# Performance work log

Hardware: AMD Instinct MI355X
Metric: run time of the kernel (lower is better)

The kernel has to match this reference:

```python
import jax, jax.numpy as jnp
import numpy as np


def setup_inputs() -> dict:
    key = jax.random.key(0)
    ks = jax.random.split(key, 7)
    B, T, C, H = 4, 4096, 1024, 64
    x = jax.random.normal(ks[0], (B, T, C), dtype=jnp.float32)
    Wq = jax.random.normal(ks[1], (C, H), dtype=jnp.float32) * 0.02
    bq = jax.random.normal(ks[2], (H,), dtype=jnp.float32) * 0.02
    Wk = jax.random.normal(ks[3], (C, H), dtype=jnp.float32) * 0.02
    bk = jax.random.normal(ks[4], (H,), dtype=jnp.float32) * 0.02
    Wv = jax.random.normal(ks[5], (C, H), dtype=jnp.float32) * 0.02
    bv = jax.random.normal(ks[6], (H,), dtype=jnp.float32) * 0.02
    return {"x": x, "Wq": Wq, "bq": bq, "Wk": Wk, "bk": bk, "Wv": Wv, "bv": bv}


def reference(x, Wq, bq, Wk, bk, Wv, bv):
    B, T, C = x.shape
    q = x @ Wq + bq            # [B,T,H]
    k = x @ Wk + bk            # [B,T,H]
    v = x @ Wv + bv            # [B,T,H]
    # NOTE: original scales by C**-0.5 where C = n_embd (input dim), not head_size
    scale = jnp.asarray(C, x.dtype) ** -0.5
    wei = jnp.einsum('bth,bsh->bts', q, k) * scale   # [B,T,T]
    causal = jnp.tril(jnp.ones((T, T), dtype=bool))
    wei = jnp.where(causal, wei, -jnp.inf)
    wei = jax.nn.softmax(wei, axis=-1)
    out = jnp.einsum('bts,bsh->bth', wei, v)         # [B,T,H]
    return out
```

## Files before the change

### kernel.cpp

```cpp
#include <hip/hip_runtime.h>
#include <hip/hip_bf16.h>

#define T_DIM 4096
#define C_DIM 1024
#define H_DIM 64
#define B_DIM 4

typedef __attribute__((ext_vector_type(8))) short short8v;
typedef __attribute__((ext_vector_type(4))) short short4v;
typedef __attribute__((ext_vector_type(4))) float float4v;

__device__ __forceinline__ unsigned short f2bf(float f) {
    __hip_bfloat16 h = __float2bfloat16(f);
    return *reinterpret_cast<unsigned short*>(&h);
}

__device__ __forceinline__ int vperm(int t5) {
    return ((t5 & 12) << 1) | (t5 & 3) | ((t5 & 16) >> 2);
}

#define GLL16(gsrc, ldst)                                                         \
    __builtin_amdgcn_global_load_lds(                                             \
        (const __attribute__((address_space(1))) unsigned int*)(gsrc),            \
        (__attribute__((address_space(3))) unsigned int*)(ldst), 16, 0, 0)

__global__ __launch_bounds__(256) void wprep(
    const float* __restrict__ Wq, const float* __restrict__ Wk,
    const float* __restrict__ Wv, unsigned short* __restrict__ wt)
{
    __shared__ float tile[64][65];
    const int t  = threadIdx.x;
    const int m  = blockIdx.x >> 4;
    const int k0 = (blockIdx.x & 15) * 64;
    const float* __restrict__ W = (m == 0) ? Wq : (m == 1) ? Wk : Wv;

    const int kr = t >> 4, c4 = (t & 15) * 4;
#pragma unroll
    for (int j = 0; j < 4; ++j) {
        const int row = kr + j * 16;
        const float4 v = *(const float4*)(W + (size_t)(k0 + row) * 64 + c4);
        tile[row][c4 + 0] = v.x; tile[row][c4 + 1] = v.y;
        tile[row][c4 + 2] = v.z; tile[row][c4 + 3] = v.w;
    }
    __syncthreads();

    const int col = t >> 2, q = t & 3;
    short8v s0, s1;
#pragma unroll
    for (int j = 0; j < 8; ++j) s0[j] = (short)f2bf(tile[q * 16 + j][col]);
#pragma unroll
    for (int j = 0; j < 8; ++j) s1[j] = (short)f2bf(tile[q * 16 + 8 + j][col]);
    unsigned short* dst = wt + (size_t)(m * 64 + col) * 1024 + k0 + q * 16;
    *(short8v*)dst = s0;
    *(short8v*)(dst + 8) = s1;
}

__global__ __launch_bounds__(512, 2) void qkv_gemm(
    const float* __restrict__ x, const unsigned short* __restrict__ wt,
    const float* __restrict__ bq, const float* __restrict__ bk,
    const float* __restrict__ bv,
    unsigned short* __restrict__ qb, unsigned short* __restrict__ kmat,
    unsigned short* __restrict__ vP)
{
    __shared__ __align__(16) unsigned char lx[2][4096];
    __shared__ __align__(16) unsigned char lw[2][24576];

    const int t    = threadIdx.x;
    const int lane = t & 63;
    const int w    = t >> 6;
    const int l15  = lane & 15;
    const int g4   = lane >> 4;
    const int r0   = blockIdx.x * 32;

    const int rg  = w & 1;
    const int cgr = (w >> 1) & 1;
    const int kh  = w >> 2;

    const int srow  = t >> 3;
    const int soct  = t & 7;
    const int sphys = soct ^ (srow & 7);
    const float* __restrict__ xsrc = x + (size_t)(r0 + srow) * C_DIM + soct * 8;
    const int wgs = (t & 7) ^ ((t >> 3) & 7);
    const unsigned char* __restrict__ wB = (const unsigned char*)wt;

    float4v acc[6];
#pragma unroll
    for (int cg = 0; cg < 6; ++cg) acc[cg] = (float4v){0.f, 0.f, 0.f, 0.f};

#define WSTAGE(p, kb)                                                             \
    {                                                                             \
        _Pragma("unroll")                                                         \
        for (int i = 0; i < 3; ++i)                                               \
            GLL16(wB + (size_t)(i * 64 + (t >> 3)) * 2048 + (kb) * 128 + wgs * 16,\
                  &lw[p][(i * 512 + t) * 16]);                                    \
    }

    WSTAGE(0, 0);
    if (t < 256) {
        const float4 a0 = *(const float4*)(xsrc);
        const float4 a1 = *(const float4*)(xsrc + 4);
        short8v xs;
        xs[0] = (short)f2bf(a0.x); xs[1] = (short)f2bf(a0.y);
        xs[2] = (short)f2bf(a0.z); xs[3] = (short)f2bf(a0.w);
        xs[4] = (short)f2bf(a1.x); xs[5] = (short)f2bf(a1.y);
        xs[6] = (short)f2bf(a1.z); xs[7] = (short)f2bf(a1.w);
        *(short8v*)&lx[0][srow * 128 + sphys * 16] = xs;
    }
    __syncthreads();

    const int arow = rg * 16 + l15;
    const int axor = arow & 7;
    const int kg   = kh * 4 + g4;

    for (int kb = 0; kb < 16; ++kb) {
        const int p = kb & 1;
        float4 na = {0,0,0,0}, nb = {0,0,0,0};
        if (kb < 15) {
            if (t < 256) {
                na = *(const float4*)(xsrc + (kb + 1) * 64);
                nb = *(const float4*)(xsrc + (kb + 1) * 64 + 4);
            }
            WSTAGE(p ^ 1, kb + 1);
        }

        const short8v af = *(const short8v*)&lx[p][arow * 128 + (kg ^ axor) * 16];
#pragma unroll
        for (int cg = 0; cg < 6; ++cg) {
            const int col = cgr * 96 + cg * 16 + l15;
            const short8v bf =
                *(const short8v*)&lw[p][col * 128 + ((kg ^ (col & 7))) * 16];
            acc[cg] = __builtin_amdgcn_mfma_f32_16x16x32_bf16(af, bf, acc[cg], 0, 0, 0);
        }

        if (kb < 15 && t < 256) {
            short8v xs;
            xs[0] = (short)f2bf(na.x); xs[1] = (short)f2bf(na.y);
            xs[2] = (short)f2bf(na.z); xs[3] = (short)f2bf(na.w);
            xs[4] = (short)f2bf(nb.x); xs[5] = (short)f2bf(nb.y);
            xs[6] = (short)f2bf(nb.z); xs[7] = (short)f2bf(nb.w);
            *(short8v*)&lx[p ^ 1][srow * 128 + sphys * 16] = xs;
        }
        __syncthreads();
    }

    float* comm = (float*)lw;
    if (kh == 1) {
        const int base = ((w - 4) * 64 + lane) * 24;
#pragma unroll
        for (int cg = 0; cg < 6; ++cg)
#pragma unroll
            for (int e = 0; e < 4; ++e) comm[base + cg * 4 + e] = acc[cg][e];
    }
    __syncthreads();
    if (kh == 0) {
        const int base = (w * 64 + lane) * 24;
#pragma unroll
        for (int cg = 0; cg < 6; ++cg)
#pragma unroll
            for (int e = 0; e < 4; ++e) acc[cg][e] += comm[base + cg * 4 + e];

        const float qs = 0.03125f * 1.44269504088896f;
#pragma unroll
        for (int cg = 0; cg < 6; ++cg) {
            const int cabs = cgr * 96 + cg * 16 + l15;
            const int m    = cabs >> 6;
            const int h    = cabs & 63;
            const float bb = ((m == 0) ? bq : (m == 1) ? bk : bv)[h];
#pragma unroll
            for (int rr = 0; rr < 4; ++rr) {
                const int row = r0 + rg * 16 + 4 * g4 + rr;
                const float vv = acc[cg][rr] + bb;
                if (m == 0) {
                    qb[(size_t)row * 64 + h] = f2bf(vv * qs);
                } else if (m == 1) {
                    kmat[(size_t)row * 64 + h] = f2bf(vv);
                } else {
                    const int b_i = row >> 12;
                    const int tt  = row & 4095;
                    const int tp  = (tt & ~31) | vperm(tt & 31);
                    vP[((size_t)b_i * 64 + h) * T_DIM + tp] = f2bf(vv);
                }
            }
        }
    }
#undef WSTAGE
}

__global__ __launch_bounds__(512, 4) void attn_mfma(
    const unsigned short* __restrict__ qb, const unsigned short* __restrict__ kmat,
    const unsigned short* __restrict__ vP, float* __restrict__ out)
{
    __shared__ float partO[8][32][68];
    __shared__ float partl[8][32];

    const int w    = threadIdx.x >> 6;
    const int lane = threadIdx.x & 63;
    const int l15  = lane & 15;
    const int g    = lane >> 4;
    const int i    = blockIdx.x;
    const int p2   = (i & 255) >> 2;
    const int b    = i & 3;
    const int tt   = (i < 256) ? (127 - p2) : p2;
    const int q0   = tt * 32;
    const int n    = tt + 1;

    const unsigned short* __restrict__ qbase = qb + ((size_t)b * T_DIM + q0) * 64;
    short8v qf[2][2];
    qf[0][0] = *(const short8v*)(qbase + (size_t)l15 * 64 + 8 * g);
    qf[0][1] = *(const short8v*)(qbase + (size_t)l15 * 64 + 32 + 8 * g);
    qf[1][0] = *(const short8v*)(qbase + (size_t)(16 + l15) * 64 + 8 * g);
    qf[1][1] = *(const short8v*)(qbase + (size_t)(16 + l15) * 64 + 32 + 8 * g);

    const unsigned short* __restrict__ kbase = kmat + (size_t)b * T_DIM * 64;
    const unsigned short* __restrict__ vbase = vP + (size_t)b * 64 * T_DIM;

    float4v acc[2][4];
#pragma unroll
    for (int qt = 0; qt < 2; ++qt)
#pragma unroll
        for (int f = 0; f < 4; ++f) acc[qt][f] = (float4v){0.f, 0.f, 0.f, 0.f};
    float lsum[2] = {0.f, 0.f};

    const int rem = n & 7;
    const int cnt = (n >> 3) + (w < rem ? 1 : 0);
    const int st  = w * (n >> 3) + (w < rem ? w : rem);

    for (int s = 0; s < cnt; ++s) {
        const int kv0 = (st + s) * 32;

        const unsigned short* kr0 = kbase + (size_t)(kv0 + l15) * 64 + 8 * g;
        const unsigned short* kr1 = kr0 + 16 * 64;
        const short8v ka0 = *(const short8v*)kr0;
        const short8v ka1 = *(const short8v*)(kr0 + 32);
        const short8v ka2 = *(const short8v*)kr1;
        const short8v ka3 = *(const short8v*)(kr1 + 32);

        short8v vb4[4];
#pragma unroll
        for (int f = 0; f < 4; ++f)
            vb4[f] = *(const short8v*)(
                vbase + (size_t)(f * 16 + l15) * T_DIM + kv0 + 8 * g);

#pragma unroll
        for (int qt = 0; qt < 2; ++qt) {
            const float4v z = (float4v){0.f, 0.f, 0.f, 0.f};
            float4v slo = __builtin_amdgcn_mfma_f32_16x16x32_bf16(ka0, qf[qt][0], z, 0, 0, 0);
            slo = __builtin_amdgcn_mfma_f32_16x16x32_bf16(ka1, qf[qt][1], slo, 0, 0, 0);
            float4v shi = __builtin_amdgcn_mfma_f32_16x16x32_bf16(ka2, qf[qt][0], z, 0, 0, 0);
            shi = __builtin_amdgcn_mfma_f32_16x16x32_bf16(ka3, qf[qt][1], shi, 0, 0, 0);

            short8v pa;
            float ls = 0.f;
            if (kv0 + 31 <= q0 + 16 * qt) {
#pragma unroll
                for (int r = 0; r < 4; ++r) {
                    const float plo = exp2f(slo[r]);
                    const float phi = exp2f(shi[r]);
                    pa[r]     = (short)f2bf(plo);
                    pa[4 + r] = (short)f2bf(phi);
                    ls += plo + phi;
                }
            } else {
                const int qabs = q0 + 16 * qt + l15;
#pragma unroll
                for (int r = 0; r < 4; ++r) {
                    const int kvlo = kv0 + 4 * g + r;
                    const float plo = (kvlo <= qabs) ? exp2f(slo[r]) : 0.f;
                    const float phi = (kvlo + 16 <= qabs) ? exp2f(shi[r]) : 0.f;
                    pa[r]     = (short)f2bf(plo);
                    pa[4 + r] = (short)f2bf(phi);
                    ls += plo + phi;
                }
            }
            lsum[qt] += ls;
#pragma unroll
            for (int f = 0; f < 4; ++f)
                acc[qt][f] = __builtin_amdgcn_mfma_f32_16x16x32_bf16(pa, vb4[f], acc[qt][f], 0, 0, 0);
        }
    }

#pragma unroll
    for (int qt = 0; qt < 2; ++qt) {
        lsum[qt] += __shfl_xor(lsum[qt], 16);
        lsum[qt] += __shfl_xor(lsum[qt], 32);
    }

#pragma unroll
    for (int qt = 0; qt < 2; ++qt)
#pragma unroll
        for (int f = 0; f < 4; ++f)
#pragma unroll
            for (int r = 0; r < 4; ++r)
                partO[w][16 * qt + 4 * g + r][16 * f + l15] = acc[qt][f][r];
    if (g == 0) {
        partl[w][l15]      = lsum[0];
        partl[w][16 + l15] = lsum[1];
    }
    __syncthreads();

    const int row = threadIdx.x >> 4;
    const int c0  = (threadIdx.x & 15) * 4;
    float lt = 0.f;
#pragma unroll
    for (int ww = 0; ww < 8; ++ww) lt += partl[ww][row];
    const float inv = 1.f / lt;
    float4 o = make_float4(0.f, 0.f, 0.f, 0.f);
#pragma unroll
    for (int ww = 0; ww < 8; ++ww) {
        const float4 s = *(const float4*)&partO[ww][row][c0];
        o.x += s.x; o.y += s.y; o.z += s.z; o.w += s.w;
    }
    o.x *= inv; o.y *= inv; o.z *= inv; o.w *= inv;
    *(float4*)(out + ((size_t)b * T_DIM + q0 + row) * 64 + c0) = o;
}

extern "C" void kernel_launch(void* const* d_in, const int* in_sizes, int n_in,
                              void* d_out, int out_size, void* d_ws, size_t ws_size,
                              hipStream_t stream) {
    const float* x  = (const float*)d_in[0];
    const float* Wq = (const float*)d_in[1];
    const float* bq = (const float*)d_in[2];
    const float* Wk = (const float*)d_in[3];
    const float* bk = (const float*)d_in[4];
    const float* Wv = (const float*)d_in[5];
    const float* bv = (const float*)d_in[6];
    float* out = (float*)d_out;

    const size_t rows = (size_t)B_DIM * T_DIM;
    char* ws = (char*)d_ws;
    unsigned short* qb   = (unsigned short*)ws;
    unsigned short* kmat = qb + rows * H_DIM;
    unsigned short* vP   = kmat + rows * H_DIM;
    unsigned short* wt   = vP + rows * H_DIM;

    wprep<<<48, 256, 0, stream>>>(Wq, Wk, Wv, wt);
    qkv_gemm<<<512, 512, 0, stream>>>(x, wt, bq, bk, bv, qb, kmat, vP);
    attn_mfma<<<512, 512, 0, stream>>>(qb, kmat, vP, out);
}
```

Measured before the change: 63.02 us.

## Pipeline x loads in projection with all threads; compute softmax row sums via MFMA

The projection kernel now has all 512 threads load and convert x in float4 pieces. It prefetches two k-steps ahead with alternating registers, uses packed bf16 conversions and replaces __syncthreads with explicit waitcnt/barrier plus sched_barriers. The k-loop is fully unrolled and the last iteration is peeled. In the attention kernel, the per-row probability sum moves from scalar adds plus cross-lane shuffles to an extra MFMA against a ones vector, and the probabilities are packed with paired bf16 conversion. The aim is more overlap of memory latency and fewer VALU instructions, at the cost of one more MFMA per tile and row sums taken from bf16-rounded probabilities, which changes numerics slightly.

```diff
diff --git a/kernel.cpp b/kernel.cpp
--- a/kernel.cpp
+++ b/kernel.cpp
@@ -76,10 +76,10 @@
     const int cgr = (w >> 1) & 1;
     const int kh  = w >> 2;
 
-    const int srow  = t >> 3;
-    const int soct  = t & 7;
-    const int sphys = soct ^ (srow & 7);
-    const float* __restrict__ xsrc = x + (size_t)(r0 + srow) * C_DIM + soct * 8;
+    const int srow  = t >> 4;
+    const int sq    = t & 15;
+    const int xbyte = srow * 128 + ((sq >> 1) ^ (srow & 7)) * 16 + (sq & 1) * 8;
+    const float* __restrict__ xsrc = x + (size_t)(r0 + srow) * C_DIM + sq * 4;
     const int wgs = (t & 7) ^ ((t >> 3) & 7);
     const unsigned char* __restrict__ wB = (const unsigned char*)wt;
 
@@ -94,34 +94,40 @@
             GLL16(wB + (size_t)(i * 64 + (t >> 3)) * 2048 + (kb) * 128 + wgs * 16,\
                   &lw[p][(i * 512 + t) * 16]);                                    \
     }
-
-    WSTAGE(0, 0);
-    if (t < 256) {
-        const float4 a0 = *(const float4*)(xsrc);
-        const float4 a1 = *(const float4*)(xsrc + 4);
-        short8v xs;
-        xs[0] = (short)f2bf(a0.x); xs[1] = (short)f2bf(a0.y);
-        xs[2] = (short)f2bf(a0.z); xs[3] = (short)f2bf(a0.w);
-        xs[4] = (short)f2bf(a1.x); xs[5] = (short)f2bf(a1.y);
-        xs[6] = (short)f2bf(a1.z); xs[7] = (short)f2bf(a1.w);
-        *(short8v*)&lx[0][srow * 128 + sphys * 16] = xs;
-    }
-    __syncthreads();
+#define XCVT_WRITE(p, v)                                                          \
+    {                                                                             \
+        __hip_bfloat162 c0_ = __float22bfloat162_rn(make_float2((v).x, (v).y));   \
+        __hip_bfloat162 c1_ = __float22bfloat162_rn(make_float2((v).z, (v).w));   \
+        unsigned int* d_ = (unsigned int*)&lx[p][xbyte];                          \
+        d_[0] = *(unsigned int*)&c0_;                                             \
+        d_[1] = *(unsigned int*)&c1_;                                             \
+    }
+
+    float4 xvA, xvB;
+
+    {
+        const float4 x0 = *(const float4*)xsrc;
+        WSTAGE(0, 0);
+        __builtin_amdgcn_sched_barrier(0);
+        xvA = *(const float4*)(xsrc + 64);
+        XCVT_WRITE(0, x0);
+        asm volatile("s_waitcnt vmcnt(1) lgkmcnt(0)" ::: "memory");
+        __builtin_amdgcn_s_barrier();
+        __builtin_amdgcn_sched_barrier(0);
+    }
 
     const int arow = rg * 16 + l15;
     const int axor = arow & 7;
     const int kg   = kh * 4 + g4;
 
-    for (int kb = 0; kb < 16; ++kb) {
+#pragma unroll
+    for (int kb = 0; kb < 15; ++kb) {
         const int p = kb & 1;
-        float4 na = {0,0,0,0}, nb = {0,0,0,0};
-        if (kb < 15) {
-            if (t < 256) {
-                na = *(const float4*)(xsrc + (kb + 1) * 64);
-                nb = *(const float4*)(xsrc + (kb + 1) * 64 + 4);
-            }
-            WSTAGE(p ^ 1, kb + 1);
-        }
+        WSTAGE(p ^ 1, kb + 1);
+        __builtin_amdgcn_sched_barrier(0);
+        const int pf = (kb + 2 < 16) ? (kb + 2) : 15;
+        if ((kb & 1) == 0) xvB = *(const float4*)(xsrc + pf * 64);
+        else               xvA = *(const float4*)(xsrc + pf * 64);
 
         const short8v af = *(const short8v*)&lx[p][arow * 128 + (kg ^ axor) * 16];
 #pragma unroll
@@ -132,16 +138,24 @@
             acc[cg] = __builtin_amdgcn_mfma_f32_16x16x32_bf16(af, bf, acc[cg], 0, 0, 0);
         }
 
-        if (kb < 15 && t < 256) {
-            short8v xs;
-            xs[0] = (short)f2bf(na.x); xs[1] = (short)f2bf(na.y);
-            xs[2] = (short)f2bf(na.z); xs[3] = (short)f2bf(na.w);
-            xs[4] = (short)f2bf(nb.x); xs[5] = (short)f2bf(nb.y);
-            xs[6] = (short)f2bf(nb.z); xs[7] = (short)f2bf(nb.w);
-            *(short8v*)&lx[p ^ 1][srow * 128 + sphys * 16] = xs;
+        if ((kb & 1) == 0) { XCVT_WRITE(p ^ 1, xvA); }
+        else               { XCVT_WRITE(p ^ 1, xvB); }
+
+        asm volatile("s_waitcnt vmcnt(1) lgkmcnt(0)" ::: "memory");
+        __builtin_amdgcn_s_barrier();
+        __builtin_amdgcn_sched_barrier(0);
+    }
+    {
+        const short8v af = *(const short8v*)&lx[1][arow * 128 + (kg ^ axor) * 16];
+#pragma unroll
+        for (int cg = 0; cg < 6; ++cg) {
+            const int col = cgr * 96 + cg * 16 + l15;
+            const short8v bf =
+                *(const short8v*)&lw[1][col * 128 + ((kg ^ (col & 7))) * 16];
+            acc[cg] = __builtin_amdgcn_mfma_f32_16x16x32_bf16(af, bf, acc[cg], 0, 0, 0);
         }
-        __syncthreads();
-    }
+    }
+    __syncthreads();
 
     float* comm = (float*)lw;
     if (kh == 1) {
@@ -184,6 +198,7 @@
         }
     }
 #undef WSTAGE
+#undef XCVT_WRITE
 }
 
 __global__ __launch_bounds__(512, 4) void attn_mfma(
@@ -214,12 +229,18 @@
     const unsigned short* __restrict__ kbase = kmat + (size_t)b * T_DIM * 64;
     const unsigned short* __restrict__ vbase = vP + (size_t)b * 64 * T_DIM;
 
+    short8v kones;
+#pragma unroll
+    for (int j = 0; j < 8; ++j) kones[j] = (short)0x3F80;
+
     float4v acc[2][4];
-#pragma unroll
-    for (int qt = 0; qt < 2; ++qt)
+    float4v accl[2];
+#pragma unroll
+    for (int qt = 0; qt < 2; ++qt) {
 #pragma unroll
         for (int f = 0; f < 4; ++f) acc[qt][f] = (float4v){0.f, 0.f, 0.f, 0.f};
-    float lsum[2] = {0.f, 0.f};
+        accl[qt] = (float4v){0.f, 0.f, 0.f, 0.f};
+    }
 
     const int rem = n & 7;
     const int cnt = (n >> 3) + (w < rem ? 1 : 0);
@@ -249,40 +270,39 @@
             float4v shi = __builtin_amdgcn_mfma_f32_16x16x32_bf16(ka2, qf[qt][0], z, 0, 0, 0);
             shi = __builtin_amdgcn_mfma_f32_16x16x32_bf16(ka3, qf[qt][1], shi, 0, 0, 0);
 
-            short8v pa;
-            float ls = 0.f;
+            float pl[4], ph[4];
             if (kv0 + 31 <= q0 + 16 * qt) {
 #pragma unroll
                 for (int r = 0; r < 4; ++r) {
-                    const float plo = exp2f(slo[r]);
-                    const float phi = exp2f(shi[r]);
-                    pa[r]     = (short)f2bf(plo);
-                    pa[4 + r] = (short)f2bf(phi);
-                    ls += plo + phi;
+                    pl[r] = exp2f(slo[r]);
+                    ph[r] = exp2f(shi[r]);
                 }
             } else {
                 const int qabs = q0 + 16 * qt + l15;
 #pragma unroll
                 for (int r = 0; r < 4; ++r) {
                     const int kvlo = kv0 + 4 * g + r;
-                    const float plo = (kvlo <= qabs) ? exp2f(slo[r]) : 0.f;
-                    const float phi = (kvlo + 16 <= qabs) ? exp2f(shi[r]) : 0.f;
-                    pa[r]     = (short)f2bf(plo);
-                    pa[4 + r] = (short)f2bf(phi);
-                    ls += plo + phi;
+                    pl[r] = (kvlo <= qabs) ? exp2f(slo[r]) : 0.f;
+                    ph[r] = (kvlo + 16 <= qabs) ? exp2f(shi[r]) : 0.f;
                 }
             }
-            lsum[qt] += ls;
+            short8v pa;
+            {
+                unsigned int* pu = (unsigned int*)&pa;
+                __hip_bfloat162 c0 = __float22bfloat162_rn(make_float2(pl[0], pl[1]));
+                __hip_bfloat162 c1 = __float22bfloat162_rn(make_float2(pl[2], pl[3]));
+                __hip_bfloat162 c2 = __float22bfloat162_rn(make_float2(ph[0], ph[1]));
+                __hip_bfloat162 c3 = __float22bfloat162_rn(make_float2(ph[2], ph[3]));
+                pu[0] = *(unsigned int*)&c0;
+                pu[1] = *(unsigned int*)&c1;
+                pu[2] = *(unsigned int*)&c2;
+                pu[3] = *(unsigned int*)&c3;
+            }
 #pragma unroll
             for (int f = 0; f < 4; ++f)
                 acc[qt][f] = __builtin_amdgcn_mfma_f32_16x16x32_bf16(pa, vb4[f], acc[qt][f], 0, 0, 0);
+            accl[qt] = __builtin_amdgcn_mfma_f32_16x16x32_bf16(pa, kones, accl[qt], 0, 0, 0);
         }
-    }
-
-#pragma unroll
-    for (int qt = 0; qt < 2; ++qt) {
-        lsum[qt] += __shfl_xor(lsum[qt], 16);
-        lsum[qt] += __shfl_xor(lsum[qt], 32);
     }
 
 #pragma unroll
@@ -292,9 +312,12 @@
 #pragma unroll
             for (int r = 0; r < 4; ++r)
                 partO[w][16 * qt + 4 * g + r][16 * f + l15] = acc[qt][f][r];
-    if (g == 0) {
-        partl[w][l15]      = lsum[0];
-        partl[w][16 + l15] = lsum[1];
+    if (l15 == 0) {
+#pragma unroll
+        for (int qt = 0; qt < 2; ++qt)
+#pragma unroll
+            for (int r = 0; r < 4; ++r)
+                partl[w][16 * qt + 4 * g + r] = accl[qt][r];
     }
     __syncthreads();
 
```

New measurement: 62.00 us. Within noise of the previous version (-1.6%).
